# Kernel tuning notes

Hardware: AMD Instinct MI355X
Metric: run time of the kernel (lower is better)

Reference implementation:

```python
import jax, jax.numpy as jnp
import numpy as np

# NTU RGB+D 25-joint skeleton edges (1-based)
NTU_EDGES = [(1,2),(2,21),(3,21),(4,3),(5,21),(6,5),(7,6),(8,7),(9,21),(10,9),
             (11,10),(12,11),(13,1),(14,13),(15,14),(16,15),(17,1),(18,17),
             (19,18),(20,19),(22,23),(23,8),(24,25),(25,12)]
NUM_SCALES = 13
NUM_POINT = 25


def build_A_powers(num_scales=NUM_SCALES, v=NUM_POINT):
    # MS-G3D disentangled multi-scale aggregation: exact-k-hop adjacencies, each
    # with self loops, symmetrically normalized, stacked along dim 0 -> (K*V, V).
    A = np.zeros((v, v))
    for i, j in NTU_EDGES:
        A[i - 1, j - 1] = 1.0
        A[j - 1, i - 1] = 1.0
    I = np.eye(v)
    mats = []
    for k in range(num_scales):
        if k == 0:
            Ak = I.copy()
        else:
            Ak = np.minimum(np.linalg.matrix_power(A + I, k), 1) \
               - np.minimum(np.linalg.matrix_power(A + I, k - 1), 1)
            Ak = Ak + I  # with_self=True
        d = Ak.sum(-1)
        dinv = np.where(d > 0, d ** -0.5, 0.0)
        mats.append((dinv[:, None] * Ak) * dinv[None, :])
    return np.concatenate(mats, 0).astype(np.float32)


def batchnorm(x, g, b, axes, ch_axis, eps=1e-5):
    # torch BatchNorm in training mode: biased batch stats + affine
    mean = jnp.mean(x, axes, keepdims=True)
    var = jnp.mean((x - mean) ** 2, axes, keepdims=True)
    shape = [1] * x.ndim
    shape[ch_axis] = -1
    return (x - mean) * jax.lax.rsqrt(var + eps) * g.reshape(shape) + b.reshape(shape)


def ms_gcn(x, A_powers, A_res, W, b, g, beta, num_scales):
    # x: (N, C, T, V); A: (K*V, V)
    A = A_powers + A_res
    support = jnp.einsum('vu,nctu->nctv', A, x)            # (N, C, T, K*V)
    N, C, T, KV = support.shape
    V = KV // num_scales
    support = support.reshape(N, C, T, num_scales, V).transpose(0, 3, 1, 2, 4)
    support = support.reshape(N, num_scales * C, T, V)     # (N, K*C, T, V)
    out = jnp.einsum('oc,nctv->notv', W, support) + b[None, :, None, None]  # 1x1 conv
    out = batchnorm(out, g, beta, (0, 2, 3), 1)
    return jax.nn.relu(out)


def lstm(x, Wih, Whh, bih, bhh):
    # single-layer batch_first LSTM, zero initial state; torch gate order i,f,g,o
    B = x.shape[0]
    H = Whh.shape[1]
    xp = jnp.einsum('bsd,hd->bsh', x, Wih) + bih + bhh     # precompute input proj

    def step(carry, xt):
        h, c = carry
        gates = xt + h @ Whh.T
        i, f, g, o = jnp.split(gates, 4, axis=-1)
        c = jax.nn.sigmoid(f) * c + jax.nn.sigmoid(i) * jnp.tanh(g)
        h = jax.nn.sigmoid(o) * jnp.tanh(c)
        return (h, c), h

    init = (jnp.zeros((B, H), x.dtype), jnp.zeros((B, H), x.dtype))
    _, ys = jax.lax.scan(step, init, jnp.swapaxes(xp, 0, 1))
    return jnp.swapaxes(ys, 0, 1)                          # (B, S, H)


def logsig_rnn(x, n_segments, Wih, Whh, bih, bhh):
    # x: (B, T, d). Depth-2 log-signature per time segment + segment start point,
    # concatenated and fed to an LSTM (Logsig-RNN layer).
    B, T, d = x.shape
    t_vec = np.array([int(round(float(v))) for v in np.linspace(1, T, n_segments + 1)])
    starts = t_vec[:-1] - 1
    ends = t_vec[1:] - 1
    L = int((ends - starts).max()) + 1
    # pad segments to fixed length by repeating the last point (zero increments)
    idx = np.minimum(starts[:, None] + np.arange(L)[None, :], ends[:, None])  # (S, L)
    pts = x[:, idx, :]                                     # (B, S, L, d)
    rel = pts - pts[:, :, :1, :]
    inc = rel[:, :, -1, :]                                 # level-1: total increment
    dx = pts[:, :, 1:, :] - pts[:, :, :-1, :]
    Mm = jnp.einsum('bsli,bslj->bsij', rel[:, :, :-1, :], dx)
    iu, ju = np.triu_indices(d, k=1)
    levy = 0.5 * (Mm[:, :, iu, ju] - Mm[:, :, ju, iu])     # level-2 (Lyndon basis)
    feats = jnp.concatenate([x[:, starts, :], inc, levy], axis=-1)
    return lstm(feats, Wih, Whh, bih, bhh)


def setup_inputs() -> dict:
    key = jax.random.key(0)
    ks = iter(jax.random.split(key, 16))
    N, C, T, V, M = 2, 3, 100, 25, 2
    c1, c2, num_class, K = 96, 192, 60, NUM_SCALES

    def randn(shape, scale):
        return jax.random.normal(next(ks), shape, jnp.float32) * scale

    ls1 = c1 + c1 * (c1 - 1) // 2     # 4656
    ls2 = c2 + c2 * (c2 - 1) // 2     # 18528
    in1 = c1 + ls1                    # 4752
    in2 = c2 + ls2                    # 18720
    Ap = jnp.asarray(build_A_powers())
    return {
        'x': jax.random.normal(next(ks), (N, C, T, V, M), jnp.float32),
        'length': jax.random.randint(next(ks), (N,), 0, T),
        'data_bn_g': jnp.ones((M * V * C,)), 'data_bn_b': jnp.zeros((M * V * C,)),
        'A_powers1': Ap,
        'A_res1': jax.random.uniform(next(ks), Ap.shape, jnp.float32, -1e-6, 1e-6),
        'W1': randn((c1, K * C), (K * C) ** -0.5), 'b1': jnp.zeros((c1,)),
        'bn1_g': jnp.ones((c1,)), 'bn1_b': jnp.zeros((c1,)),
        'Wih1': randn((4 * c1, in1), in1 ** -0.5), 'Whh1': randn((4 * c1, c1), c1 ** -0.5),
        'bih1': jnp.zeros((4 * c1,)), 'bhh1': jnp.zeros((4 * c1,)),
        'bnseg1_g': jnp.ones((50,)), 'bnseg1_b': jnp.zeros((50,)),
        'A_powers2': Ap,
        'A_res2': jax.random.uniform(next(ks), Ap.shape, jnp.float32, -1e-6, 1e-6),
        'W2': randn((c2, K * c1), (K * c1) ** -0.5), 'b2': jnp.zeros((c2,)),
        'bn2_g': jnp.ones((c2,)), 'bn2_b': jnp.zeros((c2,)),
        'Wih2': randn((4 * c2, in2), in2 ** -0.5), 'Whh2': randn((4 * c2, c2), c2 ** -0.5),
        'bih2': jnp.zeros((4 * c2,)), 'bhh2': jnp.zeros((4 * c2,)),
        'bnseg2_g': jnp.ones((30,)), 'bnseg2_b': jnp.zeros((30,)),
        'fcW': randn((num_class, c2), c2 ** -0.5), 'fcb': jnp.zeros((num_class,)),
    }


def reference(x, length, data_bn_g, data_bn_b, A_powers1, A_res1, W1, b1, bn1_g, bn1_b,
              Wih1, Whh1, bih1, bhh1, bnseg1_g, bnseg1_b, A_powers2, A_res2, W2, b2,
              bn2_g, bn2_b, Wih2, Whh2, bih2, bhh2, bnseg2_g, bnseg2_b, fcW, fcb):
    # `length` is accepted but unused, as in the original forward.
    N, C, T, V, M = x.shape
    K = A_powers1.shape[0] // V
    c1, c2 = W1.shape[0], W2.shape[0]
    S1, S2 = 50, 30

    h = x.transpose(0, 4, 3, 1, 2).reshape(N, M * V * C, T)
    h = batchnorm(h, data_bn_g, data_bn_b, (0, 2), 1)
    h = h.reshape(N * M, V, C, T).transpose(0, 2, 3, 1)            # (NM, C, T, V)

    h = jax.nn.relu(ms_gcn(h, A_powers1, A_res1, W1, b1, bn1_g, bn1_b, K))
    h = h.transpose(0, 3, 2, 1).reshape(N * M * V, T, c1)
    h = logsig_rnn(h, S1, Wih1, Whh1, bih1, bhh1)                  # (NMV, S1, c1)
    h = batchnorm(h, bnseg1_g, bnseg1_b, (0, 2), 1)
    h = h.reshape(N * M, V, S1, c1).transpose(0, 3, 2, 1)          # (NM, c1, S1, V)

    h = jax.nn.relu(ms_gcn(h, A_powers2, A_res2, W2, b2, bn2_g, bn2_b, K))
    h = h.transpose(0, 3, 2, 1).reshape(N * M * V, S1, c2)
    h = logsig_rnn(h, S2, Wih2, Whh2, bih2, bhh2)                  # (NMV, S2, c2)
    h = batchnorm(h, bnseg2_g, bnseg2_b, (0, 2), 1)
    h = h.reshape(N * M, V, S2, c2).transpose(0, 3, 2, 1)          # (NM, c2, S2, V)

    pooled = h.reshape(N, M, c2, -1).mean(axis=3).mean(axis=1)     # (N, c2)
    return pooled @ fcW.T + fcb
```

## Files before the change

### kernel.cpp

```cpp
#include <hip/hip_runtime.h>
#include <cmath>
#include <cstdint>
#include <cstddef>

typedef unsigned short bf16_t;
typedef __attribute__((ext_vector_type(8))) short short8;
typedef __attribute__((ext_vector_type(4))) float floatx4;
typedef __attribute__((ext_vector_type(2))) _Float16 half2_t;
typedef __attribute__((ext_vector_type(8))) _Float16 half8_t;

__device__ __forceinline__ float bf2f(bf16_t b){
  unsigned int u = ((unsigned int)b) << 16;
  return __uint_as_float(u);
}
__device__ __forceinline__ bf16_t f2bf(float f){
  unsigned int u = __float_as_uint(f);
  unsigned int r = (u + 0x7fffu + ((u >> 16) & 1u)) >> 16;
  return (bf16_t)r;
}
__device__ __forceinline__ unsigned int f2bf2(float a, float b){
  return (unsigned int)f2bf(a) | ((unsigned int)f2bf(b) << 16);
}
__device__ __forceinline__ float sigf(float x){ return 1.0f / (1.0f + expf(-x)); }

__device__ __forceinline__ float dot2(half2_t a, half2_t b, float c){
#if __has_builtin(__builtin_amdgcn_fdot2)
  return __builtin_amdgcn_fdot2(a, b, c, false);
#else
  return c + (float)a.x * (float)b.x + (float)a.y * (float)b.y;
#endif
}

__device__ __forceinline__ void gload_lds16(const bf16_t* g, bf16_t* lds){
  __builtin_amdgcn_global_load_lds(
      (const __attribute__((address_space(1))) unsigned int*)g,
      (__attribute__((address_space(3))) unsigned int*)lds, 16, 0, 0);
}

__device__ __forceinline__ void barrier_raw(){
  asm volatile("s_barrier" ::: "memory");
}

__device__ __forceinline__ int xcd_chunk_swizzle(int orig, int nwg){
  int q = nwg >> 3, r = nwg & 7;
  int xcd = orig & 7, idx = orig >> 3;
  return (xcd < r ? xcd * (q + 1) : r * (q + 1) + (xcd - r) * q) + idx;
}

__global__ void prep_misc(const float* __restrict__ a1, const float* __restrict__ r1, float* __restrict__ o1,
                          const float* __restrict__ a2, const float* __restrict__ r2, float* __restrict__ o2,
                          const float* __restrict__ bi1, const float* __restrict__ bh1, float* __restrict__ ob1,
                          const float* __restrict__ bi2, const float* __restrict__ bh2, float* __restrict__ ob2,
                          const float* __restrict__ Whh1, half2_t* __restrict__ Wp1,
                          const float* __restrict__ Whh2, half2_t* __restrict__ Wp2,
                          unsigned short* __restrict__ lut1, unsigned short* __restrict__ lut2,
                          float* __restrict__ stats, bf16_t* __restrict__ A2mat){
  int i = blockIdx.x * blockDim.x + threadIdx.x;
  if (i < 8125){ o1[i] = a1[i] + r1[i]; o2[i] = a2[i] + r2[i]; }
  if (i < 384) ob1[i] = bi1[i] + bh1[i];
  if (i < 768) ob2[i] = bi2[i] + bh2[i];
  if (i < 736) stats[i] = 0.f;
  if (i < 18432){
    int t = i % 384, j2 = i / 384;
    half2_t w; w.x = (_Float16)Whh1[(size_t)t * 96 + 2 * j2];
    w.y = (_Float16)Whh1[(size_t)t * 96 + 2 * j2 + 1];
    Wp1[i] = w;
  }
  if (i < 73728){
    int t = i % 768, j2 = i / 768;
    half2_t w; w.x = (_Float16)Whh2[(size_t)t * 192 + 2 * j2];
    w.y = (_Float16)Whh2[(size_t)t * 192 + 2 * j2 + 1];
    Wp2[i] = w;
  }
  if (i < 4560){
    int d = 96, p = i;
    int r = (int)(((2.0 * d - 1.0) - sqrt((2.0 * d - 1.0) * (2.0 * d - 1.0) - 8.0 * (double)p)) * 0.5);
    if (r < 0) r = 0;
    while (r + 1 <= d - 2 && (r + 1) * (d - 1) - ((r + 1) * r) / 2 <= p) ++r;
    while (r > 0 && r * (d - 1) - (r * (r - 1)) / 2 > p) --r;
    int jj = p - (r * (d - 1) - (r * (r - 1)) / 2);
    lut1[p] = (unsigned short)((r << 8) | (r + 1 + jj));
  }
  if (i < 18336){
    int d = 192, p = i;
    int r = (int)(((2.0 * d - 1.0) - sqrt((2.0 * d - 1.0) * (2.0 * d - 1.0) - 8.0 * (double)p)) * 0.5);
    if (r < 0) r = 0;
    while (r + 1 <= d - 2 && (r + 1) * (d - 1) - ((r + 1) * r) / 2 <= p) ++r;
    while (r > 0 && r * (d - 1) - (r * (r - 1)) / 2 > p) --r;
    int jj = p - (r * (d - 1) - (r * (r - 1)) / 2);
    lut2[p] = (unsigned short)((r << 8) | (r + 1 + jj));
  }
  if (i < 160000){
    int row = i >> 5, col = 1248 + (i & 31);
    A2mat[(size_t)row * 1280 + col] = 0;
  }
}

__device__ __forceinline__ void f2bf_seg(const float* in, bf16_t* out, int Kin, int Kout, int li){
  int ko8 = Kout >> 3;
  int r = li / ko8, k8 = (li % ko8) << 3;
  uint4 u;
  if (k8 + 8 <= Kin){
    const float4* p = reinterpret_cast<const float4*>(in + (size_t)r * Kin + k8);
    float4 x0 = p[0], x1 = p[1];
    u.x = f2bf2(x0.x, x0.y); u.y = f2bf2(x0.z, x0.w);
    u.z = f2bf2(x1.x, x1.y); u.w = f2bf2(x1.z, x1.w);
  } else {
    u.x = u.y = u.z = u.w = 0u;
  }
  *reinterpret_cast<uint4*>(out + (size_t)r * Kout + k8) = u;
}

__global__ void f2bf_pad8_3(const float* __restrict__ in1, bf16_t* __restrict__ out1, int Kin1, int Kout1, int c1,
                            const float* __restrict__ in2, bf16_t* __restrict__ out2, int Kin2, int Kout2, int c2,
                            const float* __restrict__ in3, bf16_t* __restrict__ out3, int Kin3, int Kout3, int c3){
  int idx = blockIdx.x * blockDim.x + threadIdx.x;
  if (idx < c1){ f2bf_seg(in1, out1, Kin1, Kout1, idx); return; }
  idx -= c1;
  if (idx < c2){ f2bf_seg(in2, out2, Kin2, Kout2, idx); return; }
  idx -= c2;
  if (idx < c3) f2bf_seg(in3, out3, Kin3, Kout3, idx);
}

__global__ void data_bn_kernel(const float* __restrict__ x, const float* __restrict__ g,
                               const float* __restrict__ bb, float* __restrict__ h1,
                               int N, int C, int T, int V, int M){
  int ch = blockIdx.x;
  int m = ch / (V * C);
  int v = (ch / C) % V;
  int c = ch % C;
  int tid = threadIdx.x;
  int cnt = N * T;
  float s = 0.f, s2 = 0.f;
  for (int i = tid; i < cnt; i += 64){
    int n = i / T, t = i % T;
    float val = x[(((size_t)(n * C + c) * T + t) * V + v) * M + m];
    s += val; s2 += val * val;
  }
  for (int off = 32; off; off >>= 1){ s += __shfl_down(s, off); s2 += __shfl_down(s2, off); }
  s = __shfl(s, 0); s2 = __shfl(s2, 0);
  float mean = s / cnt;
  float rstd = rsqrtf(s2 / cnt - mean * mean + 1e-5f);
  float gg = g[ch], bo = bb[ch];
  for (int i = tid; i < cnt; i += 64){
    int n = i / T, t = i % T;
    float val = x[(((size_t)(n * C + c) * T + t) * V + v) * M + m];
    float y = (val - mean) * rstd * gg + bo;
    h1[((size_t)((n * M + m) * C + c) * T + t) * V + v] = y;
  }
}

__global__ __launch_bounds__(256)
void gcn1_fused(const float* __restrict__ A, const float* __restrict__ h1,
                const float* __restrict__ W1, const float* __restrict__ b1,
                float* __restrict__ y1, float* __restrict__ ssum, float* __restrict__ ssq, int T){
  __shared__ float h[3][25];
  __shared__ float sup[3][325];
  __shared__ float lsum[96], lsq[96];
  int blk = blockIdx.x;
  int nm = blk / T, t = blk % T;
  int tid = threadIdx.x;
  if (tid < 75){
    int c = tid / 25, v = tid % 25;
    h[c][v] = h1[((size_t)(nm * 3 + c) * T + t) * 25 + v];
  }
  if (tid < 96){ lsum[tid] = 0.f; lsq[tid] = 0.f; }
  __syncthreads();
  for (int w = tid; w < 975; w += 256){
    int c = w / 325, ww = w % 325;
    const float* ar = A + ww * 25;
    float acc = 0.f;
    #pragma unroll
    for (int u = 0; u < 25; ++u) acc += ar[u] * h[c][u];
    sup[c][ww] = acc;
  }
  __syncthreads();
  for (int o2 = tid; o2 < 2400; o2 += 256){
    int v = o2 / 96, o = o2 % 96;
    float acc = b1[o];
    #pragma unroll
    for (int k = 0; k < 13; ++k)
      #pragma unroll
      for (int c = 0; c < 3; ++c)
        acc += W1[o * 39 + k * 3 + c] * sup[c][k * 25 + v];
    y1[((size_t)blk * 25 + v) * 96 + o] = acc;
    atomicAdd(&lsum[o], acc);
    atomicAdd(&lsq[o], acc * acc);
  }
  __syncthreads();
  if (tid < 96){ atomicAdd(&ssum[tid], lsum[tid]); atomicAdd(&ssq[tid], lsq[tid]); }
}

struct SegTable { int st[50]; int en[50]; };

__global__ void feats_bn_kernel(const float* __restrict__ ymat, const float* __restrict__ sum,
                                const float* __restrict__ sumsq, const float* __restrict__ g,
                                const float* __restrict__ bb, bf16_t* __restrict__ feats,
                                SegTable segs, const unsigned int* __restrict__ lut32,
                                int T, int d, int S, int L, int pairs, int rowlenP, int R){
  __shared__ float pts[4][192];
  int bs = blockIdx.x;
  int b = bs / S, s = bs % S;
  int nm = b / 25, v = b % 25;
  int st = segs.st[s], en = segs.en[s];
  int nt = blockDim.x, tid = threadIdx.x;
  for (int l = 0; l < L; ++l){
    int t = st + l; if (t > en) t = en;
    const float* yrow = ymat + ((size_t)(nm * T + t) * 25 + v) * d;
    for (int i = tid; i < d; i += nt){
      float mean = sum[i] / R;
      float rstd = rsqrtf(sumsq[i] / R - mean * mean + 1e-5f);
      pts[l][i] = fmaxf((yrow[i] - mean) * rstd * g[i] + bb[i], 0.f);
    }
  }
  __syncthreads();
  unsigned int* frow32 = reinterpret_cast<unsigned int*>(feats + (size_t)bs * rowlenP);
  int d2 = d >> 1;
  for (int i2 = tid; i2 < d2; i2 += nt){
    int i = 2 * i2;
    frow32[i2]      = f2bf2(pts[0][i], pts[0][i + 1]);
    frow32[d2 + i2] = f2bf2(pts[L - 1][i] - pts[0][i], pts[L - 1][i + 1] - pts[0][i + 1]);
  }
  int rowlen2 = (2 * d + pairs) >> 1, rowlenP2 = rowlenP >> 1;
  for (int i = tid + rowlen2; i < rowlenP2; i += nt) frow32[i] = 0;
  int Lm2 = L - 2;
  unsigned int* lrow32 = frow32 + d;
  int pairs2 = pairs >> 1;
  for (int p2 = tid; p2 < pairs2; p2 += nt){
    unsigned int ee = lut32[p2];
    int i0 = (ee >> 8) & 255, j0 = ee & 255;
    int i1 = ee >> 24, j1 = (ee >> 16) & 255;
    float acc0 = 0.f, acc1 = 0.f;
    for (int l = 1; l <= Lm2; ++l){
      float ri = pts[l][i0] - pts[0][i0], rj = pts[l][j0] - pts[0][j0];
      float di = pts[l + 1][i0] - pts[l][i0], dj = pts[l + 1][j0] - pts[l][j0];
      acc0 += ri * dj - rj * di;
      float ri1 = pts[l][i1] - pts[0][i1], rj1 = pts[l][j1] - pts[0][j1];
      float di1 = pts[l + 1][i1] - pts[l][i1], dj1 = pts[l + 1][j1] - pts[l][j1];
      acc1 += ri1 * dj1 - rj1 * di1;
    }
    lrow32[p2] = f2bf2(0.5f * acc0, 0.5f * acc1);
  }
}

__global__ __launch_bounds__(256)
void gemm_mfma_nt_split(const bf16_t* __restrict__ A, const bf16_t* __restrict__ B,
                        float* __restrict__ P, int M, int N, int K,
                        int GX, int GY, int GZ){
  __shared__ bf16_t As[128 * 64];
  __shared__ bf16_t Bs[128 * 64];
  const int nwg = GX * GY * GZ;
  const int wg = xcd_chunk_swizzle(blockIdx.x, nwg);
  const int bxi = wg % GX, byi = (wg / GX) % GY, bzi = wg / (GX * GY);
  const int tid = threadIdx.x;
  const int lane = tid & 63, wv = tid >> 6;
  const int bm = bxi * 128, bn = byi * 128;
  const int wr = (wv >> 1) * 64, wc = (wv & 1) * 64;
  const int m_l = lane & 15, q = lane >> 4;

  const int ksteps = K >> 6;
  const int Z = GZ, z = bzi;
  const int per = (ksteps + Z - 1) / Z;
  const int ks0 = z * per;
  const int ks1 = (ks0 + per < ksteps) ? ks0 + per : ksteps;

  const int rlane = lane >> 3;
  const int slane = lane & 7;
  const int colc = (slane ^ rlane) * 8;
  const bf16_t* gA[4]; const bf16_t* gB[4];
  bf16_t* lA[4]; bf16_t* lB[4];
  #pragma unroll
  for (int it = 0; it < 4; ++it){
    int c = it * 4 + wv;
    int rowA = bm + c * 8 + rlane; if (rowA > M - 1) rowA = M - 1;
    int rowB = bn + c * 8 + rlane; if (rowB > N - 1) rowB = N - 1;
    gA[it] = A + (size_t)rowA * K + colc;
    gB[it] = B + (size_t)rowB * K + colc;
    lA[it] = &As[c * 512];
    lB[it] = &Bs[c * 512];
  }
  const int sxor = m_l & 7;

  floatx4 acc[4][4] = {};
  for (int ks = ks0; ks < ks1; ++ks){
    int k0 = ks << 6;
    __syncthreads();
    #pragma unroll
    for (int it = 0; it < 4; ++it){
      gload_lds16(gA[it] + k0, lA[it]);
      gload_lds16(gB[it] + k0, lB[it]);
    }
    __syncthreads();
    #pragma unroll
    for (int half = 0; half < 2; ++half){
      const int scol = ((half * 4 + q) ^ sxor) * 8;
      short8 af[4], bfr[4];
      #pragma unroll
      for (int i = 0; i < 4; ++i){
        af[i]  = *reinterpret_cast<const short8*>(&As[(wr + i * 16 + m_l) * 64 + scol]);
        bfr[i] = *reinterpret_cast<const short8*>(&Bs[(wc + i * 16 + m_l) * 64 + scol]);
      }
      #pragma unroll
      for (int mi = 0; mi < 4; ++mi)
        #pragma unroll
        for (int ni = 0; ni < 4; ++ni)
          acc[mi][ni] = __builtin_amdgcn_mfma_f32_16x16x32_bf16(af[mi], bfr[ni], acc[mi][ni], 0, 0, 0);
    }
  }

  float* Pz = P + (size_t)z * M * N;
  #pragma unroll
  for (int mi = 0; mi < 4; ++mi){
    int row0 = bm + wr + mi * 16 + q * 4;
    #pragma unroll
    for (int r = 0; r < 4; ++r){
      int row = row0 + r;
      if (row < M){
        #pragma unroll
        for (int ni = 0; ni < 4; ++ni){
          int col = bn + wc + ni * 16 + m_l;
          if (col < N) Pz[(size_t)row * N + col] = acc[mi][ni][r];
        }
      }
    }
  }
}

#define VMC4 asm volatile("s_waitcnt vmcnt(4)" ::: "memory")
#define VMC0 asm volatile("s_waitcnt vmcnt(0)" ::: "memory")
#define STG4(NB, KH, OFF) { gload_lds16(pA0 + (OFF) + (KH) * 32, dA0 + (NB) * 16384 + (KH) * 8192); \
                            gload_lds16(pA1 + (OFF) + (KH) * 32, dA1 + (NB) * 16384 + (KH) * 8192); \
                            gload_lds16(pB0 + (OFF) + (KH) * 32, dB0 + (NB) * 16384 + (KH) * 8192); \
                            gload_lds16(pB1 + (OFF) + (KH) * 32, dB1 + (NB) * 16384 + (KH) * 8192); }
#define HP(BUF, KH, STAGE_BLOCK, WAIT_BLOCK) { \
    const bf16_t* ab_ = As + (BUF) * 16384 + (KH) * 8192 + sA; \
    _Pragma("unroll") \
    for (int i_ = 0; i_ < 8; ++i_) af[i_] = *reinterpret_cast<const short8*>(ab_ + i_ * 512); \
    const bf16_t* bb_ = Bs + (BUF) * 16384 + (KH) * 8192 + sB; \
    _Pragma("unroll") \
    for (int i_ = 0; i_ < 4; ++i_) bfr[i_] = *reinterpret_cast<const short8*>(bb_ + i_ * 512); \
    STAGE_BLOCK; \
    WAIT_BLOCK; \
    barrier_raw(); \
    __builtin_amdgcn_s_setprio(1); \
    _Pragma("unroll") \
    for (int mi_ = 0; mi_ < 8; ++mi_) \
      _Pragma("unroll") \
      for (int ni_ = 0; ni_ < 4; ++ni_) \
        acc[mi_][ni_] = __builtin_amdgcn_mfma_f32_16x16x32_bf16(af[mi_], bfr[ni_], acc[mi_][ni_], 0, 0, 0); \
    __builtin_amdgcn_s_setprio(0); \
  }

__global__ __launch_bounds__(512, 2)
void gemm_mfma_nt_8ph(const bf16_t* __restrict__ A, const bf16_t* __restrict__ B,
                      float* __restrict__ P, int M, int N, int K,
                      int GX, int GY, int GZ){
  __shared__ bf16_t As[32768];
  __shared__ bf16_t Bs[32768];
  const int nwg = GX * GY * GZ;
  const int wg = xcd_chunk_swizzle(blockIdx.x, nwg);
  const int bxi = wg % GX, byi = (wg / GX) % GY, bzi = wg / (GX * GY);
  const int tid = threadIdx.x;
  const int lane = tid & 63, wv = tid >> 6;
  const int wm = wv >> 2, wn = wv & 3;
  const int m_l = lane & 15, q = lane >> 4;
  const int bm = bxi * 256, bn = byi * 256;

  const int ksteps = K >> 6;
  const int z = bzi, Z = GZ;
  const int per = (ksteps + Z - 1) / Z;
  const int ks0 = z * per;
  int ks1 = ks0 + per; if (ks1 > ksteps) ks1 = ksteps;
  if (ks0 >= ks1) return;

  const int rlane = lane >> 2, slane = lane & 3;
  const int cg = slane ^ ((rlane >> 1) & 3);
  int rr0 = wv * 16 + rlane, rr1 = (8 + wv) * 16 + rlane;
  int ra0 = bm + rr0; if (ra0 > M - 1) ra0 = M - 1;
  int ra1 = bm + rr1; if (ra1 > M - 1) ra1 = M - 1;
  int rb0 = bn + rr0; if (rb0 > N - 1) rb0 = N - 1;
  int rb1 = bn + rr1; if (rb1 > N - 1) rb1 = N - 1;
  const bf16_t* pA0 = A + (size_t)ra0 * K + cg * 8 + ks0 * 64;
  const bf16_t* pA1 = A + (size_t)ra1 * K + cg * 8 + ks0 * 64;
  const bf16_t* pB0 = B + (size_t)rb0 * K + cg * 8 + ks0 * 64;
  const bf16_t* pB1 = B + (size_t)rb1 * K + cg * 8 + ks0 * 64;
  bf16_t* dA0 = As + wv * 512;
  bf16_t* dA1 = As + (8 + wv) * 512;
  bf16_t* dB0 = Bs + wv * 512;
  bf16_t* dB1 = Bs + (8 + wv) * 512;

  const int sA = (wm * 128 + m_l) * 32 + ((q ^ ((m_l >> 1) & 3)) * 8);
  const int sB = (wn * 64 + m_l) * 32 + ((q ^ ((m_l >> 1) & 3)) * 8);

  short8 af[8], bfr[4];
  floatx4 acc[8][4] = {};

  STG4(0, 0, 0); STG4(0, 1, 0);
  VMC4;
  barrier_raw();

  int buf = 0;
  for (int t = ks0; t < ks1 - 1; ++t){
    const int nb = buf ^ 1;
    HP(buf, 0, STG4(nb, 0, 64), VMC4);
    HP(buf, 1, STG4(nb, 1, 64), VMC4);
    pA0 += 64; pA1 += 64; pB0 += 64; pB1 += 64;
    buf = nb;
  }
  HP(buf, 0, ((void)0), VMC0);
  HP(buf, 1, ((void)0), ((void)0));

  float* Pz = P + (size_t)z * M * N;
  #pragma unroll
  for (int mi = 0; mi < 8; ++mi){
    int row0 = bm + wm * 128 + mi * 16 + q * 4;
    #pragma unroll
    for (int r = 0; r < 4; ++r){
      int row = row0 + r;
      if (row < M){
        #pragma unroll
        for (int ni = 0; ni < 4; ++ni){
          int col = bn + wn * 64 + ni * 16 + m_l;
          if (col < N) Pz[(size_t)row * N + col] = acc[mi][ni][r];
        }
      }
    }
  }
}

__global__ __launch_bounds__(256)
void reduce_split_bias_stats(const float* __restrict__ P, const float* __restrict__ bias,
                             float* __restrict__ out, float* __restrict__ ssum, float* __restrict__ ssq,
                             int MN, int N, int Z){
  __shared__ float lsum[192], lsq[192];
  int tid = threadIdx.x;
  if (tid < 192){ lsum[tid] = 0.f; lsq[tid] = 0.f; }
  __syncthreads();
  int i4 = (blockIdx.x * blockDim.x + tid) * 4;
  if (i4 < MN){
    const float4 bv = *reinterpret_cast<const float4*>(bias + (i4 % N));
    float4 s = bv;
    for (int z = 0; z < Z; ++z){
      const float4 p = *reinterpret_cast<const float4*>(P + (size_t)z * MN + i4);
      s.x += p.x; s.y += p.y; s.z += p.z; s.w += p.w;
    }
    *reinterpret_cast<float4*>(out + i4) = s;
    int c0 = i4 % N;
    atomicAdd(&lsum[c0],     s.x); atomicAdd(&lsq[c0],     s.x * s.x);
    atomicAdd(&lsum[c0 + 1], s.y); atomicAdd(&lsq[c0 + 1], s.y * s.y);
    atomicAdd(&lsum[c0 + 2], s.z); atomicAdd(&lsq[c0 + 2], s.z * s.z);
    atomicAdd(&lsum[c0 + 3], s.w); atomicAdd(&lsq[c0 + 3], s.w * s.w);
  }
  __syncthreads();
  if (tid < 192){ atomicAdd(&ssum[tid], lsum[tid]); atomicAdd(&ssq[tid], lsq[tid]); }
}

template <int H2C, int BLK, int Z>
__global__ __launch_bounds__(BLK, 1)
void lstm_kernel(const float* __restrict__ P, const float* __restrict__ bias,
                 const half2_t* __restrict__ Wp, float* __restrict__ out,
                 float* __restrict__ ssum, float* __restrict__ ssq,
                 int S, int MN){
  constexpr int H = 2 * H2C;
  constexpr int H4 = 4 * H;
  __shared__ _Float16 __attribute__((aligned(16))) hsh[H];
  __shared__ float gv[H4];
  __shared__ float ra[BLK / 64], rb[BLK / 64];
  const int b = blockIdx.x, t = threadIdx.x;
  const int lane = t & 63, wid = t >> 6;
  half2_t w[H2C];
  const half2_t* wp = Wp + t;
  #pragma unroll
  for (int j2 = 0; j2 < H2C; ++j2) w[j2] = wp[(size_t)j2 * H4];
  float cc = 0.f;
  if (t < H) hsh[t] = (_Float16)0.f;
  const float bval = bias[t];
  const size_t base = (size_t)b * S * H4 + t;
  float pv0[Z], pv1[Z];
  #pragma unroll
  for (int z = 0; z < Z; ++z) pv0[z] = P[(size_t)z * MN + base];
  #pragma unroll
  for (int z = 0; z < Z; ++z) pv1[z] = P[(size_t)z * MN + base + H4];
  __syncthreads();
  const half8_t* hp8 = reinterpret_cast<const half8_t*>(hsh);
  for (int s = 0; s < S; ++s){
    float pvn[Z];
    if (s + 2 < S){
      size_t o2 = base + (size_t)(s + 2) * H4;
      #pragma unroll
      for (int z = 0; z < Z; ++z) pvn[z] = P[(size_t)z * MN + o2];
    }
    float a0 = bval, a1 = 0.f, a2 = 0.f, a3 = 0.f;
    float a4 = 0.f, a5 = 0.f, a6 = 0.f, a7 = 0.f;
    #pragma unroll
    for (int z = 0; z < Z; ++z) a0 += pv0[z];
    #pragma unroll
    for (int j8 = 0; j8 < H2C / 8; ++j8){
      half8_t hv0 = hp8[2 * j8];
      half8_t hv1 = hp8[2 * j8 + 1];
      half2_t h0, h1, h2, h3, h4, h5, h6, h7;
      h0.x = hv0[0]; h0.y = hv0[1];
      h1.x = hv0[2]; h1.y = hv0[3];
      h2.x = hv0[4]; h2.y = hv0[5];
      h3.x = hv0[6]; h3.y = hv0[7];
      h4.x = hv1[0]; h4.y = hv1[1];
      h5.x = hv1[2]; h5.y = hv1[3];
      h6.x = hv1[4]; h6.y = hv1[5];
      h7.x = hv1[6]; h7.y = hv1[7];
      const int jb = 8 * j8;
      a0 = dot2(w[jb],     h0, a0);
      a1 = dot2(w[jb + 1], h1, a1);
      a2 = dot2(w[jb + 2], h2, a2);
      a3 = dot2(w[jb + 3], h3, a3);
      a4 = dot2(w[jb + 4], h4, a4);
      a5 = dot2(w[jb + 5], h5, a5);
      a6 = dot2(w[jb + 6], h6, a6);
      a7 = dot2(w[jb + 7], h7, a7);
    }
    gv[t] = ((a0 + a1) + (a2 + a3)) + ((a4 + a5) + (a6 + a7));
    __syncthreads();
    float gvv = 0.f;
    if (t < H){
      float ig = sigf(gv[t]);
      float fg = sigf(gv[H + t]);
      float gg = tanhf(gv[2 * H + t]);
      float og = sigf(gv[3 * H + t]);
      cc = fg * cc + ig * gg;
      float hh = og * tanhf(cc);
      hsh[t] = (_Float16)hh;
      out[((size_t)b * S + s) * H + t] = hh;
      gvv = hh;
    }
    float q1 = gvv, q2 = gvv * gvv;
    for (int off2 = 32; off2; off2 >>= 1){ q1 += __shfl_down(q1, off2); q2 += __shfl_down(q2, off2); }
    if (lane == 0){ ra[wid] = q1; rb[wid] = q2; }
    __syncthreads();
    if (t == 0){
      float sa = 0.f, sb = 0.f;
      #pragma unroll
      for (int ww = 0; ww < BLK / 64; ++ww){ sa += ra[ww]; sb += rb[ww]; }
      atomicAdd(&ssum[s], sa);
      atomicAdd(&ssq[s], sb);
    }
    #pragma unroll
    for (int z = 0; z < Z; ++z){ pv0[z] = pv1[z]; pv1[z] = pvn[z]; }
  }
}

__global__ void support2_bn(const float* __restrict__ A, const float* __restrict__ lout,
                            const float* __restrict__ ssum, const float* __restrict__ ssq,
                            const float* __restrict__ g, const float* __restrict__ bb,
                            bf16_t* __restrict__ A2mat, int S, int cnt){
  int idx = blockIdx.x * blockDim.x + threadIdx.x;
  int total = 4 * S * 25 * 13 * 96;
  if (idx >= total) return;
  int c = idx % 96;
  int k = (idx / 96) % 13;
  int v = (idx / (96 * 13)) % 25;
  int rs = idx / (96 * 13 * 25);
  int s = rs % S, nm = rs / S;
  float mean = ssum[s] / cnt;
  float rstd = rsqrtf(ssq[s] / cnt - mean * mean + 1e-5f);
  float scale = rstd * g[s];
  float shift = bb[s] - mean * scale;
  const float* ar = A + (k * 25 + v) * 25;
  float acc = 0.f;
  #pragma unroll
  for (int u = 0; u < 25; ++u){
    float raw = lout[((size_t)(nm * 25 + u) * S + s) * 96 + c];
    acc += ar[u] * (raw * scale + shift);
  }
  A2mat[((size_t)rs * 25 + v) * 1280 + k * 96 + c] = f2bf(acc);
}

__global__ void pool_kernel(const float* __restrict__ lout2, const float* __restrict__ sum,
                            const float* __restrict__ sumsq, const float* __restrict__ g,
                            const float* __restrict__ bb, float* __restrict__ pooled,
                            int S, int H, int scnt){
  int n = blockIdx.x / H;
  int o = blockIdx.x % H;
  float acc = 0.f;
  int cnt = 2 * 25 * S;
  for (int i = threadIdx.x; i < cnt; i += 64){
    int m = i / (25 * S);
    int r = i % (25 * S);
    int v = r / S;
    int s = r % S;
    int b = (n * 2 + m) * 25 + v;
    float val = lout2[((size_t)b * S + s) * H + o];
    float mean = sum[s] / scnt;
    float rstd = rsqrtf(sumsq[s] / scnt - mean * mean + 1e-5f);
    val = (val - mean) * rstd * g[s] + bb[s];
    acc += val;
  }
  for (int off = 32; off; off >>= 1) acc += __shfl_down(acc, off);
  if (threadIdx.x == 0) pooled[n * H + o] = acc / cnt;
}

__global__ void fc_kernel(const float* __restrict__ pooled, const float* __restrict__ fcW,
                          const float* __restrict__ fcb, float* __restrict__ outp){
  int idx = blockIdx.x * blockDim.x + threadIdx.x;
  if (idx >= 120) return;
  int n = idx / 60, cls = idx % 60;
  float acc = fcb[cls];
  for (int o = 0; o < 192; ++o) acc += pooled[n * 192 + o] * fcW[cls * 192 + o];
  outp[idx] = acc;
}

static void make_segs(int T, int S, SegTable& tab, int& L){
  double step = (double)(T - 1) / (double)S;
  long long tv[51];
  for (int i = 0; i <= S; ++i){
    double v = 1.0 + step * (double)i;
    tv[i] = llrint(v);
  }
  L = 0;
  for (int s = 0; s < S; ++s){
    tab.st[s] = (int)tv[s] - 1;
    tab.en[s] = (int)tv[s + 1] - 1;
    int len = tab.en[s] - tab.st[s] + 1;
    if (len > L) L = len;
  }
  for (int s = S; s < 50; ++s){ tab.st[s] = 0; tab.en[s] = 0; }
  if (L > 4) L = 4;
}

extern "C" void kernel_launch(void* const* d_in, const int* in_sizes, int n_in,
                              void* d_out, int out_size, void* d_ws, size_t ws_size,
                              hipStream_t stream){
  const float* x         = (const float*)d_in[0];
  const float* data_bn_g = (const float*)d_in[2];
  const float* data_bn_b = (const float*)d_in[3];
  const float* A_powers1 = (const float*)d_in[4];
  const float* A_res1    = (const float*)d_in[5];
  const float* W1        = (const float*)d_in[6];
  const float* b1        = (const float*)d_in[7];
  const float* bn1_g     = (const float*)d_in[8];
  const float* bn1_b     = (const float*)d_in[9];
  const float* Wih1      = (const float*)d_in[10];
  const float* Whh1      = (const float*)d_in[11];
  const float* bih1      = (const float*)d_in[12];
  const float* bhh1      = (const float*)d_in[13];
  const float* bnseg1_g  = (const float*)d_in[14];
  const float* bnseg1_b  = (const float*)d_in[15];
  const float* A_powers2 = (const float*)d_in[16];
  const float* A_res2    = (const float*)d_in[17];
  const float* W2        = (const float*)d_in[18];
  const float* b2        = (const float*)d_in[19];
  const float* bn2_g     = (const float*)d_in[20];
  const float* bn2_b     = (const float*)d_in[21];
  const float* Wih2      = (const float*)d_in[22];
  const float* Whh2      = (const float*)d_in[23];
  const float* bih2      = (const float*)d_in[24];
  const float* bhh2      = (const float*)d_in[25];
  const float* bnseg2_g  = (const float*)d_in[26];
  const float* bnseg2_b  = (const float*)d_in[27];
  const float* fcW       = (const float*)d_in[28];
  const float* fcb       = (const float*)d_in[29];
  float* out = (float*)d_out;

  const int N = 2, C = 3, T = 100, V = 25, M = 2, NM = 4;
  const int C1 = 96, C2 = 192;
  const int S1 = 50, S2 = 30;
  const int B = 100;
  const int IN1 = 4752, IN2 = 18720;
  const int IN1P = 4800, IN2P = 18752;
  const int P1 = 4560, P2 = 18336;
  const int KG2 = 1248, KG2P = 1280;
  const int Z1 = 6, Z2 = 7, ZG = 4;

  size_t off = 0;
  char* base = (char*)d_ws;
  auto alloc = [&](size_t nbytes) -> void* {
    off = (off + 255) & ~(size_t)255;
    void* p = base + off;
    off += nbytes;
    return p;
  };
  float* A1full = (float*)alloc(325 * 25 * 4);
  float* A2full = (float*)alloc(325 * 25 * 4);
  float* h1     = (float*)alloc((size_t)NM * C * T * V * 4);
  float* y1mat  = (float*)alloc((size_t)NM * T * V * C1 * 4);
  float* stats  = (float*)alloc(736 * 4);
  float* st1a = stats, *st1b = stats + 96;
  float* sg1a = stats + 192, *sg1b = stats + 242;
  float* st2a = stats + 292, *st2b = stats + 484;
  float* sg2a = stats + 676, *sg2b = stats + 706;
  float* l1out  = (float*)alloc((size_t)B * S1 * C1 * 4);
  bf16_t* A2mat = (bf16_t*)alloc((size_t)NM * S1 * V * KG2P * 2);
  float* y2mat  = (float*)alloc((size_t)NM * S1 * V * C2 * 4);
  float* l2out  = (float*)alloc((size_t)B * S2 * C2 * 4);
  float* pooled = (float*)alloc(2 * C2 * 4);
  float* bias1  = (float*)alloc(4 * C1 * 4);
  float* bias2  = (float*)alloc(4 * C2 * 4);
  half2_t* Wp1  = (half2_t*)alloc((size_t)(C1 / 2) * 4 * C1 * 4);
  half2_t* Wp2  = (half2_t*)alloc((size_t)(C2 / 2) * 4 * C2 * 4);
  bf16_t* Wih1b = (bf16_t*)alloc((size_t)4 * C1 * IN1P * 2);
  bf16_t* Wih2b = (bf16_t*)alloc((size_t)4 * C2 * IN2P * 2);
  bf16_t* W2b   = (bf16_t*)alloc((size_t)C2 * KG2P * 2);
  unsigned short* lut1 = (unsigned short*)alloc((size_t)P1 * 2);
  unsigned short* lut2 = (unsigned short*)alloc((size_t)P2 * 2);
  size_t pmax = (size_t)Z2 * 3000 * 768;
  {
    size_t p1s = (size_t)Z1 * 5000 * 384; if (p1s > pmax) pmax = p1s;
    size_t pgs = (size_t)ZG * 5000 * 192; if (pgs > pmax) pmax = pgs;
  }
  float* Pbuf = (float*)alloc(pmax * 4);
  bf16_t* feats = (bf16_t*)alloc((size_t)B * S2 * IN2P * 2);
  (void)ws_size; (void)in_sizes; (void)n_in; (void)out_size;

  prep_misc<<<625, 256, 0, stream>>>(A_powers1, A_res1, A1full, A_powers2, A_res2, A2full,
                                     bih1, bhh1, bias1, bih2, bhh2, bias2,
                                     Whh1, Wp1, Whh2, Wp2, lut1, lut2, stats, A2mat);
  {
    int c1 = 4 * C1 * (IN1P / 8);
    int c2 = 4 * C2 * (IN2P / 8);
    int c3 = C2 * (KG2P / 8);
    int tot = c1 + c2 + c3;
    f2bf_pad8_3<<<(tot + 255) / 256, 256, 0, stream>>>(Wih1, Wih1b, IN1, IN1P, c1,
                                                       Wih2, Wih2b, IN2, IN2P, c2,
                                                       W2, W2b, KG2, KG2P, c3);
  }

  data_bn_kernel<<<M * V * C, 64, 0, stream>>>(x, data_bn_g, data_bn_b, h1, N, C, T, V, M);

  gcn1_fused<<<NM * T, 256, 0, stream>>>(A1full, h1, W1, b1, y1mat, st1a, st1b, T);

  SegTable seg1, seg2; int L1, L2;
  make_segs(T, S1, seg1, L1);
  make_segs(S1, S2, seg2, L2);

  feats_bn_kernel<<<B * S1, 256, 0, stream>>>(y1mat, st1a, st1b, bn1_g, bn1_b, feats, seg1,
                                              (const unsigned int*)lut1, T, C1, S1, L1, P1, IN1P,
                                              NM * T * 25);
  {
    int Mm = B * S1, Nn = 4 * C1;
    int GX = (Mm + 255) / 256, GY = (Nn + 255) / 256;
    gemm_mfma_nt_8ph<<<GX * GY * Z1, 512, 0, stream>>>(feats, Wih1b, Pbuf, Mm, Nn, IN1P,
                                                       GX, GY, Z1);
    lstm_kernel<48, 384, Z1><<<B, 384, 0, stream>>>(Pbuf, bias1, Wp1, l1out, sg1a, sg1b, S1, Mm * Nn);
  }

  {
    int tot = NM * S1 * 25 * 13 * 96;
    support2_bn<<<(tot + 255) / 256, 256, 0, stream>>>(A2full, l1out, sg1a, sg1b, bnseg1_g,
                                                       bnseg1_b, A2mat, S1, B * C1);
  }
  {
    int Mm = NM * S1 * 25, Nn = C2;
    int GX = (Mm + 127) / 128, GY = (Nn + 127) / 128;
    gemm_mfma_nt_split<<<GX * GY * ZG, 256, 0, stream>>>(A2mat, W2b, Pbuf, Mm, Nn, KG2P,
                                                         GX, GY, ZG);
    int MN = Mm * Nn;
    reduce_split_bias_stats<<<(MN / 4 + 255) / 256, 256, 0, stream>>>(Pbuf, b2, y2mat, st2a, st2b,
                                                                      MN, Nn, ZG);
  }

  feats_bn_kernel<<<B * S2, 256, 0, stream>>>(y2mat, st2a, st2b, bn2_g, bn2_b, feats, seg2,
                                              (const unsigned int*)lut2, S1, C2, S2, L2, P2, IN2P,
                                              NM * S1 * 25);
  {
    int Mm = B * S2, Nn = 4 * C2;
    int GX = (Mm + 255) / 256, GY = (Nn + 255) / 256;
    gemm_mfma_nt_8ph<<<GX * GY * Z2, 512, 0, stream>>>(feats, Wih2b, Pbuf, Mm, Nn, IN2P,
                                                       GX, GY, Z2);
    lstm_kernel<96, 768, Z2><<<B, 768, 0, stream>>>(Pbuf, bias2, Wp2, l2out, sg2a, sg2b, S2, Mm * Nn);
  }

  pool_kernel<<<2 * C2, 64, 0, stream>>>(l2out, sg2a, sg2b, bnseg2_g, bnseg2_b, pooled, S2, C2, B * C2);
  fc_kernel<<<1, 128, 0, stream>>>(pooled, fcW, fcb, out);
}
```

Baseline: 641.2 us.

## Parallelize LSTM gate activations and move per-step BN stats to separate kernel

In the LSTM recurrence, every thread now applies its own gate nonlinearity into shared memory, instead of the first H threads computing all four gate activations serially. The per-step reduction of segment BatchNorm statistics (shuffle reduction plus atomics) is removed from the sequential loop. A new kernel computes those sums after the LSTM finishes, with plain stores instead of atomics. This shortens the serial critical path of each timestep. The cost is an extra barrier per step and an extra kernel launch that re-reads the LSTM output.

```diff
diff --git a/kernel.cpp b/kernel.cpp
--- a/kernel.cpp
+++ b/kernel.cpp
@@ -459,15 +459,13 @@
 __global__ __launch_bounds__(BLK, 1)
 void lstm_kernel(const float* __restrict__ P, const float* __restrict__ bias,
                  const half2_t* __restrict__ Wp, float* __restrict__ out,
-                 float* __restrict__ ssum, float* __restrict__ ssq,
                  int S, int MN){
   constexpr int H = 2 * H2C;
   constexpr int H4 = 4 * H;
   __shared__ _Float16 __attribute__((aligned(16))) hsh[H];
   __shared__ float gv[H4];
-  __shared__ float ra[BLK / 64], rb[BLK / 64];
+  __shared__ float av[H4];
   const int b = blockIdx.x, t = threadIdx.x;
-  const int lane = t & 63, wid = t >> 6;
   half2_t w[H2C];
   const half2_t* wp = Wp + t;
   #pragma unroll
@@ -519,31 +517,47 @@
     }
     gv[t] = ((a0 + a1) + (a2 + a3)) + ((a4 + a5) + (a6 + a7));
     __syncthreads();
-    float gvv = 0.f;
+    {
+      float x = gv[t];
+      av[t] = (t >= 2 * H && t < 3 * H) ? tanhf(x) : sigf(x);
+    }
+    __syncthreads();
     if (t < H){
-      float ig = sigf(gv[t]);
-      float fg = sigf(gv[H + t]);
-      float gg = tanhf(gv[2 * H + t]);
-      float og = sigf(gv[3 * H + t]);
+      float ig = av[t];
+      float fg = av[H + t];
+      float gg = av[2 * H + t];
+      float og = av[3 * H + t];
       cc = fg * cc + ig * gg;
       float hh = og * tanhf(cc);
       hsh[t] = (_Float16)hh;
       out[((size_t)b * S + s) * H + t] = hh;
-      gvv = hh;
-    }
-    float q1 = gvv, q2 = gvv * gvv;
-    for (int off2 = 32; off2; off2 >>= 1){ q1 += __shfl_down(q1, off2); q2 += __shfl_down(q2, off2); }
-    if (lane == 0){ ra[wid] = q1; rb[wid] = q2; }
+    }
     __syncthreads();
-    if (t == 0){
-      float sa = 0.f, sb = 0.f;
-      #pragma unroll
-      for (int ww = 0; ww < BLK / 64; ++ww){ sa += ra[ww]; sb += rb[ww]; }
-      atomicAdd(&ssum[s], sa);
-      atomicAdd(&ssq[s], sb);
-    }
     #pragma unroll
     for (int z = 0; z < Z; ++z){ pv0[z] = pv1[z]; pv1[z] = pvn[z]; }
+  }
+}
+
+__global__ __launch_bounds__(256)
+void seg_stats_kernel(const float* __restrict__ lout, float* __restrict__ ssum,
+                      float* __restrict__ ssq, int S, int H, int B){
+  int s = blockIdx.x;
+  int tid = threadIdx.x;
+  int cnt = B * H;
+  float a = 0.f, b2 = 0.f;
+  for (int i = tid; i < cnt; i += 256){
+    int b = i / H, o = i % H;
+    float v = lout[((size_t)b * S + s) * H + o];
+    a += v; b2 += v * v;
+  }
+  for (int off = 32; off; off >>= 1){ a += __shfl_down(a, off); b2 += __shfl_down(b2, off); }
+  __shared__ float sa[4], sb[4];
+  int wid = tid >> 6, lane = tid & 63;
+  if (lane == 0){ sa[wid] = a; sb[wid] = b2; }
+  __syncthreads();
+  if (tid == 0){
+    ssum[s] = (sa[0] + sa[1]) + (sa[2] + sa[3]);
+    ssq[s]  = (sb[0] + sb[1]) + (sb[2] + sb[3]);
   }
 }
 
@@ -738,7 +752,8 @@
     int GX = (Mm + 255) / 256, GY = (Nn + 255) / 256;
     gemm_mfma_nt_8ph<<<GX * GY * Z1, 512, 0, stream>>>(feats, Wih1b, Pbuf, Mm, Nn, IN1P,
                                                        GX, GY, Z1);
-    lstm_kernel<48, 384, Z1><<<B, 384, 0, stream>>>(Pbuf, bias1, Wp1, l1out, sg1a, sg1b, S1, Mm * Nn);
+    lstm_kernel<48, 384, Z1><<<B, 384, 0, stream>>>(Pbuf, bias1, Wp1, l1out, S1, Mm * Nn);
+    seg_stats_kernel<<<S1, 256, 0, stream>>>(l1out, sg1a, sg1b, S1, C1, B);
   }
 
   {
@@ -764,7 +779,8 @@
     int GX = (Mm + 255) / 256, GY = (Nn + 255) / 256;
     gemm_mfma_nt_8ph<<<GX * GY * Z2, 512, 0, stream>>>(feats, Wih2b, Pbuf, Mm, Nn, IN2P,
                                                        GX, GY, Z2);
-    lstm_kernel<96, 768, Z2><<<B, 768, 0, stream>>>(Pbuf, bias2, Wp2, l2out, sg2a, sg2b, S2, Mm * Nn);
+    lstm_kernel<96, 768, Z2><<<B, 768, 0, stream>>>(Pbuf, bias2, Wp2, l2out, S2, Mm * Nn);
+    seg_stats_kernel<<<S2, 256, 0, stream>>>(l2out, sg2a, sg2b, S2, C2, B);
   }
 
   pool_kernel<<<2 * C2, 64, 0, stream>>>(l2out, sg2a, sg2b, bnseg2_g, bnseg2_b, pooled, S2, C2, B * C2);
```

New measurement: 643.7 us (median of 2 runs). Within noise of the previous version (+0.4%).
